# Kernel optimization log

Hardware: AMD Instinct MI355X
Metric: run time of the kernel (lower is better)

## Reference

```python
import jax, jax.numpy as jnp
import numpy as np


def setup_inputs() -> dict:
    key = jax.random.key(0)
    k1, k2, k3, k4, k5 = jax.random.split(key, 5)
    B, S, D, F, E = 4, 4096, 1024, 2048, 8
    top_k = 2
    num_tokens = B * S
    capacity = max(int(num_tokens / E * 1.25), 4)  # 2560
    scale = 0.02
    return {
        "x": jax.random.normal(k1, (B, S, D), dtype=jnp.float32),
        "gate_w": jax.random.normal(k2, (D, E), dtype=jnp.float32) * scale,
        "w_gate": jax.random.normal(k3, (E, D, F), dtype=jnp.float32) * scale,
        "w_up": jax.random.normal(k4, (E, D, F), dtype=jnp.float32) * scale,
        "w_down": jax.random.normal(k5, (E, F, D), dtype=jnp.float32) * scale,
        "num_experts": E,
        "top_k": top_k,
        "capacity": capacity,
    }


AUX_LOSS_WEIGHT = 0.01


def reference(x, gate_w, w_gate, w_up, w_down, num_experts, top_k, capacity):
    B, S, D = x.shape
    N = B * S
    x_flat = x.reshape(N, D)

    # ---- Router ----
    logits = x_flat @ gate_w                      # [N, E]
    probs = jax.nn.softmax(logits, axis=-1)
    weights, indices = jax.lax.top_k(probs, top_k)  # [N, K]
    weights = weights / jnp.sum(weights, axis=-1, keepdims=True)

    # ---- Capacity-based dispatch ----
    indices_flat = indices.reshape(-1)            # [N*K]
    x_rep = jnp.repeat(x_flat, top_k, axis=0)     # [N*K, D]
    expert_mask = jax.nn.one_hot(indices_flat, num_experts, dtype=jnp.int32)  # [N*K, E]
    token_priority = jnp.cumsum(expert_mask, axis=0) * expert_mask
    token_rank = jnp.sum(token_priority, axis=1)  # [N*K], 1-based rank within expert
    valid = (token_rank > 0) & (token_rank <= capacity)
    gather_idx = indices_flat * capacity + (token_rank - 1)  # [N*K]

    total_slots = num_experts * capacity
    # drop-mode scatter: invalid rows are sent out-of-bounds and dropped
    safe_idx = jnp.where(valid, gather_idx, total_slots)
    dispatched = jnp.zeros((total_slots, D), dtype=x.dtype)
    dispatched = dispatched.at[safe_idx].set(x_rep, mode="drop")
    dispatched = dispatched.reshape(num_experts, capacity, D)  # [E, C, D]

    # ---- Fused experts (grouped BMM, SwiGLU) ----
    gate = jnp.einsum("ecd,edf->ecf", dispatched, w_gate)
    up = jnp.einsum("ecd,edf->ecf", dispatched, w_up)
    hidden = jax.nn.silu(gate) * up
    expert_out = jnp.einsum("ecf,efd->ecd", hidden, w_down)
    expert_out_flat = expert_out.reshape(total_slots, D)

    # ---- Combine (row-aligned gather; dropped tokens contribute zero) ----
    gathered = expert_out_flat[jnp.clip(gather_idx, 0, total_slots - 1)]
    combined = jnp.where(valid[:, None], gathered, jnp.zeros((), dtype=x.dtype))
    combined = combined.reshape(N, top_k, D)
    output = jnp.sum(combined * weights[:, :, None], axis=1)  # [N, D]

    # ---- Aux load-balance loss ----
    mask = jax.nn.one_hot(indices, num_experts, dtype=jnp.float32).sum(axis=1)  # [N, E]
    f = mask.sum(axis=0) / (N * top_k + 1e-9)
    P = probs.mean(axis=0)
    aux_loss = num_experts * jnp.sum(f * P) * AUX_LOSS_WEIGHT

    return output.reshape(B, S, D), aux_loss
```

## Files before the change

### kernel.cpp

```cpp
#include <hip/hip_runtime.h>
#include <stdint.h>

#define N_TOK 16384
#define DIM   1024
#define NEXP  8
#define FF    2048
#define CAP   2560
#define NSLOT (NEXP*CAP)

using f32x4  = __attribute__((ext_vector_type(4))) float;
using bf16x8 = __attribute__((ext_vector_type(8))) short;

__device__ __forceinline__ unsigned short f2bf(float f){
  union { float f; unsigned u; } c; c.f = f;
  unsigned u = c.u + 0x7FFFu + ((c.u >> 16) & 1u);
  return (unsigned short)(u >> 16);
}
__device__ __forceinline__ float bf2f(unsigned short h){
  union { unsigned u; float f; } c; c.u = ((unsigned)h) << 16; return c.f;
}

__device__ __forceinline__ void gld16(const unsigned short* g, unsigned short* l){
  __builtin_amdgcn_global_load_lds((__attribute__((address_space(1))) void*)(void*)g,
                                   (__attribute__((address_space(3))) void*)l,
                                   16, 0, 0);
}

#define HBAR __builtin_amdgcn_s_barrier()
#define LG0  asm volatile("s_waitcnt lgkmcnt(0)" ::: "memory")

__global__ __launch_bounds__(256) void k_router(
    const float* __restrict__ x, const float* __restrict__ gate_w,
    int* __restrict__ topidx, float* __restrict__ topw,
    float* __restrict__ wavepart)
{
  __shared__ float gwT[NEXP][DIM];
  int tid = threadIdx.x;
  for (int i = tid; i < DIM*NEXP; i += 256) gwT[i & 7][i >> 3] = gate_w[i];
  __syncthreads();
  int wave = tid >> 6, lane = tid & 63;
  int t = blockIdx.x * 4 + wave;
  const float* xr = x + (size_t)t * DIM;
  double acc[NEXP];
  #pragma unroll
  for (int e = 0; e < NEXP; e++) acc[e] = 0.0;
  for (int j = 0; j < DIM/64; j++){
    double xv = (double)xr[lane + 64*j];
    #pragma unroll
    for (int e = 0; e < NEXP; e++) acc[e] += xv * (double)gwT[e][lane + 64*j];
  }
  #pragma unroll
  for (int off = 32; off >= 1; off >>= 1){
    #pragma unroll
    for (int e = 0; e < NEXP; e++) acc[e] += __shfl_xor(acc[e], off, 64);
  }
  if (lane == 0){
    double m = acc[0];
    #pragma unroll
    for (int e = 1; e < NEXP; e++) m = fmax(m, acc[e]);
    double p[NEXP], Z = 0.0;
    #pragma unroll
    for (int e = 0; e < NEXP; e++){ p[e] = exp(acc[e] - m); Z += p[e]; }
    double invZ = 1.0 / Z;
    #pragma unroll
    for (int e = 0; e < NEXP; e++) p[e] *= invZ;
    float4* wp = (float4*)(wavepart + (size_t)t*NEXP);
    wp[0] = make_float4((float)p[0], (float)p[1], (float)p[2], (float)p[3]);
    wp[1] = make_float4((float)p[4], (float)p[5], (float)p[6], (float)p[7]);
    int i0 = 0; double p0 = p[0];
    #pragma unroll
    for (int e = 1; e < NEXP; e++) if (p[e] > p0){ p0 = p[e]; i0 = e; }
    int i1 = (i0 == 0) ? 1 : 0; double p1 = p[i1];
    #pragma unroll
    for (int e = 0; e < NEXP; e++) if (e != i0 && p[e] > p1){ p1 = p[e]; i1 = e; }
    double s = p0 + p1;
    topidx[t*2+0] = i0; topidx[t*2+1] = i1;
    topw [t*2+0] = (float)(p0/s); topw[t*2+1] = (float)(p1/s);
  }
}

__global__ __launch_bounds__(1024) void k_scan_tcv(
    const int* __restrict__ topidx, const float* __restrict__ wavepart,
    int* __restrict__ slot_token, int* __restrict__ tok_slots,
    float* __restrict__ aux_out,
    const float* __restrict__ wg, const float* __restrict__ wu, const float* __restrict__ wd,
    unsigned short* __restrict__ B1, unsigned short* __restrict__ wdT)
{
  __shared__ uint8_t smem[32768];
  const int t = threadIdx.x;

  if (blockIdx.x == 0){
    int (*sc)[NEXP] = (int(*)[NEXP])smem;
    const int base_i = t * 32;
    int ids[32];
    #pragma unroll
    for (int j = 0; j < 32; j++) ids[j] = topidx[base_i + j];
    int b[NEXP];
    #pragma unroll
    for (int e = 0; e < NEXP; e++) b[e] = 0;
    #pragma unroll
    for (int j = 0; j < 32; j++){
      #pragma unroll
      for (int e = 0; e < NEXP; e++) if (ids[j] == e) b[e]++;
    }
    #pragma unroll
    for (int e = 0; e < NEXP; e++) sc[t][e] = b[e];
    __syncthreads();
    for (int off = 1; off < 1024; off <<= 1){
      int tmp[NEXP];
      #pragma unroll
      for (int e = 0; e < NEXP; e++) tmp[e] = (t >= off) ? sc[t-off][e] : 0;
      __syncthreads();
      #pragma unroll
      for (int e = 0; e < NEXP; e++) sc[t][e] += tmp[e];
      __syncthreads();
    }
    int myb[NEXP];
    #pragma unroll
    for (int e = 0; e < NEXP; e++) myb[e] = sc[t][e] - b[e];
    int cnt[NEXP];
    #pragma unroll
    for (int e = 0; e < NEXP; e++) cnt[e] = sc[1023][e];
    #pragma unroll
    for (int j = 0; j < 32; j++){
      int slot = -1;
      #pragma unroll
      for (int e = 0; e < NEXP; e++){
        if (ids[j] == e){
          int r = myb[e]; myb[e] = r + 1;
          if (r < CAP){
            slot = e*CAP + r;
            slot_token[slot] = (base_i + j) >> 1;
          }
        }
      }
      tok_slots[base_i + j] = slot;
    }
    __syncthreads();
    float pe[NEXP];
    #pragma unroll
    for (int e = 0; e < NEXP; e++) pe[e] = 0.f;
    for (int i = t; i < N_TOK; i += 1024){
      const float4* pr = (const float4*)(wavepart + (size_t)i*NEXP);
      float4 v0 = pr[0], v1 = pr[1];
      pe[0] += v0.x; pe[1] += v0.y; pe[2] += v0.z; pe[3] += v0.w;
      pe[4] += v1.x; pe[5] += v1.y; pe[6] += v1.z; pe[7] += v1.w;
    }
    #pragma unroll
    for (int off = 32; off >= 1; off >>= 1){
      #pragma unroll
      for (int e = 0; e < NEXP; e++) pe[e] += __shfl_xor(pe[e], off, 64);
    }
    __syncthreads();
    float* scf = (float*)smem;
    const int wv = t >> 6, ln = t & 63;
    if (ln == 0){
      #pragma unroll
      for (int e = 0; e < NEXP; e++) scf[wv*NEXP + e] = pe[e];
    }
    __syncthreads();
    if (t == 0){
      float aux = 0.f;
      #pragma unroll
      for (int e = 0; e < NEXP; e++){
        float P = 0.f;
        for (int w = 0; w < 16; w++) P += scf[w*NEXP + e];
        P /= (float)N_TOK;
        float f = (float)cnt[e] / ((float)(N_TOK*2) + 1e-9f);
        aux += f * P;
      }
      aux_out[0] = (float)NEXP * aux * 0.01f;
    }
  } else {
    float (*tt)[65] = (float(*)[65])smem;
    const int bid = blockIdx.x - 1;
    const int z = bid >> 9, rem = bid & 511;
    const int mode = z >> 3, e = z & 7;
    const float* in; unsigned short* out; int R, C, ct, rt;
    if (mode < 2){
      in  = (mode == 0 ? wg : wu) + (size_t)e * DIM * FF;
      out = B1 + (size_t)e * 2 * FF * DIM;
      R = DIM; C = FF; ct = rem & 31; rt = rem >> 5;
    } else {
      in  = wd + (size_t)e * FF * DIM;
      out = wdT + (size_t)e * DIM * FF;
      R = FF; C = DIM; ct = rem >> 5; rt = rem & 31;
    }
    const int c0 = ct * 64, r0 = rt * 64;
    {
      int row = t >> 4, c4 = t & 15;
      float4 v = *(const float4*)(in + (size_t)(r0 + row)*C + c0 + c4*4);
      tt[c4*4+0][row] = v.x; tt[c4*4+1][row] = v.y;
      tt[c4*4+2][row] = v.z; tt[c4*4+3][row] = v.w;
    }
    __syncthreads();
    {
      int cl = t >> 4;
      int rs = (t & 15) * 4;
      int c  = c0 + cl;
      int orow = (mode == 0) ? ((c>>4)*32 + (c&15))
               : (mode == 1) ? ((c>>4)*32 + 16 + (c&15))
               : c;
      unsigned long long pk = 0;
      #pragma unroll
      for (int j = 0; j < 4; j++) pk |= (unsigned long long)f2bf(tt[cl][rs+j]) << (16*j);
      *(unsigned long long*)(out + (size_t)orow*R + r0 + rs) = pk;
    }
  }
}

__global__ __launch_bounds__(256) void k_gather(
    const float* __restrict__ x, const int* __restrict__ slot_token,
    unsigned short* __restrict__ disp)
{
  const int s = blockIdx.x;
  const int t = slot_token[s];
  const int tid = threadIdx.x;
  unsigned long long pk = 0ull;
  if (t >= 0){
    float4 v = *(const float4*)(x + (size_t)t*DIM + tid*4);
    pk =  (unsigned long long)f2bf(v.x)
       | ((unsigned long long)f2bf(v.y) << 16)
       | ((unsigned long long)f2bf(v.z) << 32)
       | ((unsigned long long)f2bf(v.w) << 48);
  }
  *(unsigned long long*)(disp + (size_t)s*DIM + tid*4) = pk;
}

__device__ __forceinline__ void stg(const unsigned short* gsrc, int ldg,
                                    unsigned short* Lh, int wave, int lane){
  const int sl = (lane & 3) ^ ((lane >> 3) & 3);
  #pragma unroll
  for (int j = 0; j < 2; j++){
    int bi = wave*2 + j;
    gld16(gsrc + (size_t)(bi*16 + (lane >> 2))*ldg + sl*8, Lh + bi*512);
  }
}
__device__ __forceinline__ bf16x8 frd(const unsigned short* Lh, int r, int g){
  return *(const bf16x8*)(Lh + r*32 + (((g ^ ((r >> 1) & 3))) << 3));
}
template<int MG>
__device__ __forceinline__ void mm16(f32x4 (&acc)[8][4], const bf16x8 (&a)[4], const bf16x8 (&b)[4]){
  #pragma unroll
  for (int i = 0; i < 4; i++)
    #pragma unroll
    for (int n = 0; n < 4; n++)
      acc[MG*4+i][n] = __builtin_amdgcn_mfma_f32_16x16x32_bf16(a[i], b[n], acc[MG*4+i][n], 0, 0, 0);
}

#define HALF_STEP(RS, DOSTG, VMW, ASRC, BSRC)                                   \
  {                                                                             \
    unsigned short* LA = lds + (RS)*16384;                                      \
    unsigned short* LB = LA + 8192;                                             \
    unsigned short* NS = lds + (((RS)+3)&3)*16384;                              \
    bf16x8 a[4], b[4];                                                          \
    _Pragma("unroll")                                                           \
    for (int i = 0; i < 4; i++) a[i] = frd(LA, wr*128 + i*16 + l15, g);         \
    _Pragma("unroll")                                                           \
    for (int n = 0; n < 4; n++) b[n] = frd(LB, wc*64 + n*16 + l15, g);          \
    if (DOSTG) stg(ASRC, LDG, NS, wave, lane);                                  \
    HBAR; LG0;                                                                  \
    __builtin_amdgcn_s_setprio(1);  mm16<0>(acc, a, b);                         \
    __builtin_amdgcn_s_setprio(0);                                              \
    HBAR;                                                                       \
    _Pragma("unroll")                                                           \
    for (int i = 0; i < 4; i++) a[i] = frd(LA, wr*128 + (4+i)*16 + l15, g);     \
    if (DOSTG) stg(BSRC, LDG, NS + 8192, wave, lane);                           \
    HBAR; LG0;                                                                  \
    __builtin_amdgcn_s_setprio(1);  mm16<1>(acc, a, b);                         \
    __builtin_amdgcn_s_setprio(0);                                              \
    if ((VMW) == 4) { asm volatile("s_waitcnt vmcnt(4)" ::: "memory"); }        \
    else if ((VMW) == 0) { asm volatile("s_waitcnt vmcnt(0)" ::: "memory"); }   \
    HBAR;                                                                       \
  }

template<int KDIM, int LDG, int EPI>
__global__ __launch_bounds__(512, 2) void k_gemm8(
    const unsigned short* __restrict__ A,
    const unsigned short* __restrict__ B,
    unsigned short* __restrict__ Out0,
    unsigned short* __restrict__ Out1)
{
  constexpr int NH    = KDIM / 32;
  constexpr int BROWS = (EPI == 1) ? 2*FF : DIM;
  constexpr int LDO   = (EPI == 1) ? FF : DIM;
  __shared__ unsigned short lds[65536];
  const int id = blockIdx.x;
  const int e  = id & 7;
  int t  = id >> 3;
  int ks = 0;
  if (EPI == 2){ ks = t & 1; t >>= 1; }
  const int mt = t % 10, nt = t / 10;
  const int m0 = mt*256, n0 = nt*256;
  const unsigned short* Ab = A + ((size_t)e*CAP   + m0) * LDG + (size_t)ks*KDIM;
  const unsigned short* Bb = B + ((size_t)e*BROWS + n0) * LDG + (size_t)ks*KDIM;
  const int tid = threadIdx.x, wave = tid >> 6, lane = tid & 63;
  const int wr = wave >> 2, wc = wave & 3;
  const int g = lane >> 4, l15 = lane & 15;

  f32x4 acc[8][4];
  const f32x4 z4 = {0.f,0.f,0.f,0.f};
  #pragma unroll
  for (int i = 0; i < 8; i++)
    #pragma unroll
    for (int n = 0; n < 4; n++) acc[i][n] = z4;

  stg(Ab,      LDG, lds + 0*16384,        wave, lane);
  stg(Bb,      LDG, lds + 0*16384 + 8192, wave, lane);
  stg(Ab + 32, LDG, lds + 1*16384,        wave, lane);
  stg(Bb + 32, LDG, lds + 1*16384 + 8192, wave, lane);
  stg(Ab + 64, LDG, lds + 2*16384,        wave, lane);
  stg(Bb + 64, LDG, lds + 2*16384 + 8192, wave, lane);
  asm volatile("s_waitcnt vmcnt(4)" ::: "memory");
  HBAR;

  for (int h = 0; h + 8 <= NH; h += 4){
    HALF_STEP(0, true, -1, Ab + (size_t)(h+3)*32, Bb + (size_t)(h+3)*32);
    HALF_STEP(1, true,  4, Ab + (size_t)(h+4)*32, Bb + (size_t)(h+4)*32);
    HALF_STEP(2, true, -1, Ab + (size_t)(h+5)*32, Bb + (size_t)(h+5)*32);
    HALF_STEP(3, true,  4, Ab + (size_t)(h+6)*32, Bb + (size_t)(h+6)*32);
  }
  HALF_STEP(0, true, -1, Ab + (size_t)(NH-1)*32, Bb + (size_t)(NH-1)*32);
  HALF_STEP(1, false, 0, Ab, Bb);
  HALF_STEP(2, false, -1, Ab, Bb);
  HALF_STEP(3, false, -1, Ab, Bb);

  if (EPI == 1){
    unsigned short* H = Out0 + ((size_t)e*CAP + m0 + wr*128) * (size_t)LDO;
    const int hc0 = (n0 + wc*64) >> 1;
    #pragma unroll
    for (int mf = 0; mf < 8; mf++)
      #pragma unroll
      for (int q = 0; q < 4; q++){
        int r = mf*16 + g*4 + q;
        #pragma unroll
        for (int p = 0; p < 2; p++){
          float gg = acc[mf][2*p][q], uu = acc[mf][2*p+1][q];
          float h = gg / (1.f + __expf(-gg)) * uu;
          H[(size_t)r*LDO + hc0 + p*16 + l15] = f2bf(h);
        }
      }
  } else {
    unsigned short* P = (ks ? Out1 : Out0);
    unsigned short* O = P + ((size_t)e*CAP + m0 + wr*128) * (size_t)LDO + n0 + wc*64;
    #pragma unroll
    for (int mf = 0; mf < 8; mf++)
      #pragma unroll
      for (int q = 0; q < 4; q++){
        int r = mf*16 + g*4 + q;
        #pragma unroll
        for (int n = 0; n < 4; n++)
          O[(size_t)r*LDO + n*16 + l15] = f2bf(acc[mf][n][q]);
      }
  }
}

__global__ __launch_bounds__(256) void k_combine(
    const unsigned short* __restrict__ P0, const unsigned short* __restrict__ P1,
    const int* __restrict__ tok_slots, const float* __restrict__ topw,
    float* __restrict__ out)
{
  const int t = blockIdx.x*2 + (threadIdx.x >> 7);
  const int tid = threadIdx.x & 127;
  const int s0 = tok_slots[t*2+0], s1 = tok_slots[t*2+1];
  const float w0 = topw[t*2+0], w1 = topw[t*2+1];
  float r[8];
  #pragma unroll
  for (int j = 0; j < 8; j++) r[j] = 0.f;
  if (s0 >= 0){
    bf16x8 v0 = *(const bf16x8*)(P0 + (size_t)s0*DIM + tid*8);
    bf16x8 v1 = *(const bf16x8*)(P1 + (size_t)s0*DIM + tid*8);
    #pragma unroll
    for (int j = 0; j < 8; j++)
      r[j] += w0 * (bf2f((unsigned short)v0[j]) + bf2f((unsigned short)v1[j]));
  }
  if (s1 >= 0){
    bf16x8 v0 = *(const bf16x8*)(P0 + (size_t)s1*DIM + tid*8);
    bf16x8 v1 = *(const bf16x8*)(P1 + (size_t)s1*DIM + tid*8);
    #pragma unroll
    for (int j = 0; j < 8; j++)
      r[j] += w1 * (bf2f((unsigned short)v0[j]) + bf2f((unsigned short)v1[j]));
  }
  float4* o = (float4*)(out + (size_t)t*DIM + tid*8);
  o[0] = make_float4(r[0], r[1], r[2], r[3]);
  o[1] = make_float4(r[4], r[5], r[6], r[7]);
}

extern "C" void kernel_launch(void* const* d_in, const int* in_sizes, int n_in,
                              void* d_out, int out_size, void* d_ws, size_t ws_size,
                              hipStream_t stream)
{
  const float* x      = (const float*)d_in[0];
  const float* gate_w = (const float*)d_in[1];
  const float* w_gate = (const float*)d_in[2];
  const float* w_up   = (const float*)d_in[3];
  const float* w_down = (const float*)d_in[4];
  float* out = (float*)d_out;

  uint8_t* ws = (uint8_t*)d_ws;
  int*   topidx       = (int*)ws;               ws += (size_t)N_TOK*2*4;
  float* topw         = (float*)ws;             ws += (size_t)N_TOK*2*4;
  int*   slot_token   = (int*)ws;               ws += (size_t)NSLOT*4;
  int*   tok_slots    = (int*)ws;               ws += (size_t)N_TOK*2*4;
  float* wavepart     = (float*)ws;             ws += (size_t)N_TOK*NEXP*4;
  unsigned short* disp   = (unsigned short*)ws; ws += (size_t)NSLOT*DIM*2;
  unsigned short* hidden = (unsigned short*)ws; ws += (size_t)NSLOT*FF*2;
  unsigned short* B1     = (unsigned short*)ws; ws += (size_t)NEXP*2*FF*DIM*2;
  unsigned short* wdT    = (unsigned short*)ws; ws += (size_t)NEXP*DIM*FF*2;
  size_t need = (size_t)(ws - (uint8_t*)d_ws);
  if (ws_size < need) return;
  unsigned short* P0 = disp;
  unsigned short* P1 = B1;

  hipMemsetAsync(slot_token, 0xFF, (size_t)NSLOT * sizeof(int), stream);

  k_router<<<N_TOK/4, 256, 0, stream>>>(x, gate_w, topidx, topw, wavepart);
  k_scan_tcv<<<12289, 1024, 0, stream>>>(topidx, wavepart, slot_token, tok_slots,
                                         out + (size_t)N_TOK*DIM,
                                         w_gate, w_up, w_down, B1, wdT);
  k_gather<<<NSLOT, 256, 0, stream>>>(x, slot_token, disp);
  k_gemm8<DIM, DIM, 1><<<1280, 512, 0, stream>>>(disp, B1, hidden, nullptr);
  k_gemm8<DIM, FF, 2><<<640, 512, 0, stream>>>(hidden, wdT, P0, P1);
  k_combine<<<N_TOK/2, 256, 0, stream>>>(P0, P1, tok_slots, topw, out);
}
```

Baseline: 440.8 us.

## Fuse token gather into first GEMM via indirect A loads from bf16 x

Removes the separate gather kernel and the memset. x is converted once to bf16 by extra blocks of the scan/transpose kernel, and the first expert GEMM loads A rows straight from that buffer through per-row token indices read from slot_token. Unused slots are marked -1 inside the scan block and clamped to token 0. Those rows still get computed but are never combined. This saves writing and re-reading the dispatched buffer, at the cost of scattered row loads in the GEMM A-staging path.

Measured after the change: 435.9 us. About the same (-1.1%).

```diff
diff --git a/kernel.cpp b/kernel.cpp
--- a/kernel.cpp
+++ b/kernel.cpp
@@ -84,12 +84,14 @@
     int* __restrict__ slot_token, int* __restrict__ tok_slots,
     float* __restrict__ aux_out,
     const float* __restrict__ wg, const float* __restrict__ wu, const float* __restrict__ wd,
-    unsigned short* __restrict__ B1, unsigned short* __restrict__ wdT)
+    unsigned short* __restrict__ B1, unsigned short* __restrict__ wdT,
+    const float* __restrict__ x, unsigned short* __restrict__ xb)
 {
   __shared__ uint8_t smem[32768];
   const int t = threadIdx.x;
-
-  if (blockIdx.x == 0){
+  const int bidx = blockIdx.x;
+
+  if (bidx == 0){
     int (*sc)[NEXP] = (int(*)[NEXP])smem;
     const int base_i = t * 32;
     int ids[32];
@@ -136,6 +138,10 @@
       }
       tok_slots[base_i + j] = slot;
     }
+    for (int idx = t; idx < NSLOT; idx += 1024){
+      int e2 = idx / CAP, r2 = idx - e2*CAP;
+      if (r2 >= cnt[e2]) slot_token[idx] = -1;
+    }
     __syncthreads();
     float pe[NEXP];
     #pragma unroll
@@ -171,9 +177,9 @@
       }
       aux_out[0] = (float)NEXP * aux * 0.01f;
     }
-  } else {
+  } else if (bidx <= 12288){
     float (*tt)[65] = (float(*)[65])smem;
-    const int bid = blockIdx.x - 1;
+    const int bid = bidx - 1;
     const int z = bid >> 9, rem = bid & 511;
     const int mode = z >> 3, e = z & 7;
     const float* in; unsigned short* out; int R, C, ct, rt;
@@ -206,25 +212,17 @@
       for (int j = 0; j < 4; j++) pk |= (unsigned long long)f2bf(tt[cl][rs+j]) << (16*j);
       *(unsigned long long*)(out + (size_t)orow*R + r0 + rs) = pk;
     }
-  }
-}
-
-__global__ __launch_bounds__(256) void k_gather(
-    const float* __restrict__ x, const int* __restrict__ slot_token,
-    unsigned short* __restrict__ disp)
-{
-  const int s = blockIdx.x;
-  const int t = slot_token[s];
-  const int tid = threadIdx.x;
-  unsigned long long pk = 0ull;
-  if (t >= 0){
-    float4 v = *(const float4*)(x + (size_t)t*DIM + tid*4);
-    pk =  (unsigned long long)f2bf(v.x)
-       | ((unsigned long long)f2bf(v.y) << 16)
-       | ((unsigned long long)f2bf(v.z) << 32)
-       | ((unsigned long long)f2bf(v.w) << 48);
-  }
-  *(unsigned long long*)(disp + (size_t)s*DIM + tid*4) = pk;
+  } else {
+    const int gb = bidx - 12289;
+    size_t base = ((size_t)gb*1024 + t)*4;
+    float4 v = *(const float4*)(x + base);
+    unsigned long long pk =
+        (unsigned long long)f2bf(v.x)
+      | ((unsigned long long)f2bf(v.y) << 16)
+      | ((unsigned long long)f2bf(v.z) << 32)
+      | ((unsigned long long)f2bf(v.w) << 48);
+    *(unsigned long long*)(xb + base) = pk;
+  }
 }
 
 __device__ __forceinline__ void stg(const unsigned short* gsrc, int ldg,
@@ -236,6 +234,12 @@
     gld16(gsrc + (size_t)(bi*16 + (lane >> 2))*ldg + sl*8, Lh + bi*512);
   }
 }
+__device__ __forceinline__ void stgA_ind(const unsigned short* xb, int tok0, int tok1, int k0,
+                                         unsigned short* Lh, int wave, int lane){
+  const int sl = (lane & 3) ^ ((lane >> 3) & 3);
+  gld16(xb + (size_t)tok0*DIM + k0 + sl*8, Lh + (wave*2+0)*512);
+  gld16(xb + (size_t)tok1*DIM + k0 + sl*8, Lh + (wave*2+1)*512);
+}
 __device__ __forceinline__ bf16x8 frd(const unsigned short* Lh, int r, int g){
   return *(const bf16x8*)(Lh + r*32 + (((g ^ ((r >> 1) & 3))) << 3));
 }
@@ -248,7 +252,11 @@
       acc[MG*4+i][n] = __builtin_amdgcn_mfma_f32_16x16x32_bf16(a[i], b[n], acc[MG*4+i][n], 0, 0, 0);
 }
 
-#define HALF_STEP(RS, DOSTG, VMW, ASRC, BSRC)                                   \
+#define STG_A(HH, NS)                                                           \
+  { if (EPI == 1) stgA_ind(A, tokA0, tokA1, (HH)*32, NS, wave, lane);           \
+    else          stg(Ab + (size_t)(HH)*32, LDG, NS, wave, lane); }
+
+#define HALF_STEP(RS, DOSTG, VMW, HH)                                           \
   {                                                                             \
     unsigned short* LA = lds + (RS)*16384;                                      \
     unsigned short* LB = LA + 8192;                                             \
@@ -258,14 +266,14 @@
     for (int i = 0; i < 4; i++) a[i] = frd(LA, wr*128 + i*16 + l15, g);         \
     _Pragma("unroll")                                                           \
     for (int n = 0; n < 4; n++) b[n] = frd(LB, wc*64 + n*16 + l15, g);          \
-    if (DOSTG) stg(ASRC, LDG, NS, wave, lane);                                  \
+    if (DOSTG) STG_A(HH, NS);                                                   \
     HBAR; LG0;                                                                  \
     __builtin_amdgcn_s_setprio(1);  mm16<0>(acc, a, b);                         \
     __builtin_amdgcn_s_setprio(0);                                              \
     HBAR;                                                                       \
     _Pragma("unroll")                                                           \
     for (int i = 0; i < 4; i++) a[i] = frd(LA, wr*128 + (4+i)*16 + l15, g);     \
-    if (DOSTG) stg(BSRC, LDG, NS + 8192, wave, lane);                           \
+    if (DOSTG) stg(Bb + (size_t)(HH)*32, LDG, NS + 8192, wave, lane);           \
     HBAR; LG0;                                                                  \
     __builtin_amdgcn_s_setprio(1);  mm16<1>(acc, a, b);                         \
     __builtin_amdgcn_s_setprio(0);                                              \
@@ -279,7 +287,8 @@
     const unsigned short* __restrict__ A,
     const unsigned short* __restrict__ B,
     unsigned short* __restrict__ Out0,
-    unsigned short* __restrict__ Out1)
+    unsigned short* __restrict__ Out1,
+    const int* __restrict__ slot_token)
 {
   constexpr int NH    = KDIM / 32;
   constexpr int BROWS = (EPI == 1) ? 2*FF : DIM;
@@ -298,6 +307,16 @@
   const int wr = wave >> 2, wc = wave & 3;
   const int g = lane >> 4, l15 = lane & 15;
 
+  int tokA0 = 0, tokA1 = 0;
+  if (EPI == 1){
+    int r0 = m0 + (wave*2+0)*16 + (lane >> 2);
+    int r1 = m0 + (wave*2+1)*16 + (lane >> 2);
+    int t0 = slot_token[e*CAP + r0];
+    int t1 = slot_token[e*CAP + r1];
+    tokA0 = (t0 < 0) ? 0 : t0;
+    tokA1 = (t1 < 0) ? 0 : t1;
+  }
+
   f32x4 acc[8][4];
   const f32x4 z4 = {0.f,0.f,0.f,0.f};
   #pragma unroll
@@ -305,25 +324,25 @@
     #pragma unroll
     for (int n = 0; n < 4; n++) acc[i][n] = z4;
 
-  stg(Ab,      LDG, lds + 0*16384,        wave, lane);
+  STG_A(0, lds + 0*16384);
   stg(Bb,      LDG, lds + 0*16384 + 8192, wave, lane);
-  stg(Ab + 32, LDG, lds + 1*16384,        wave, lane);
+  STG_A(1, lds + 1*16384);
   stg(Bb + 32, LDG, lds + 1*16384 + 8192, wave, lane);
-  stg(Ab + 64, LDG, lds + 2*16384,        wave, lane);
+  STG_A(2, lds + 2*16384);
   stg(Bb + 64, LDG, lds + 2*16384 + 8192, wave, lane);
   asm volatile("s_waitcnt vmcnt(4)" ::: "memory");
   HBAR;
 
   for (int h = 0; h + 8 <= NH; h += 4){
-    HALF_STEP(0, true, -1, Ab + (size_t)(h+3)*32, Bb + (size_t)(h+3)*32);
-    HALF_STEP(1, true,  4, Ab + (size_t)(h+4)*32, Bb + (size_t)(h+4)*32);
-    HALF_STEP(2, true, -1, Ab + (size_t)(h+5)*32, Bb + (size_t)(h+5)*32);
-    HALF_STEP(3, true,  4, Ab + (size_t)(h+6)*32, Bb + (size_t)(h+6)*32);
-  }
-  HALF_STEP(0, true, -1, Ab + (size_t)(NH-1)*32, Bb + (size_t)(NH-1)*32);
-  HALF_STEP(1, false, 0, Ab, Bb);
-  HALF_STEP(2, false, -1, Ab, Bb);
-  HALF_STEP(3, false, -1, Ab, Bb);
+    HALF_STEP(0, true, -1, h+3);
+    HALF_STEP(1, true,  4, h+4);
+    HALF_STEP(2, true, -1, h+5);
+    HALF_STEP(3, true,  4, h+6);
+  }
+  HALF_STEP(0, true, -1, NH-1);
+  HALF_STEP(1, false, 0, 0);
+  HALF_STEP(2, false, -1, 0);
+  HALF_STEP(3, false, -1, 0);
 
   if (EPI == 1){
     unsigned short* H = Out0 + ((size_t)e*CAP + m0 + wr*128) * (size_t)LDO;
@@ -403,23 +422,20 @@
   int*   slot_token   = (int*)ws;               ws += (size_t)NSLOT*4;
   int*   tok_slots    = (int*)ws;               ws += (size_t)N_TOK*2*4;
   float* wavepart     = (float*)ws;             ws += (size_t)N_TOK*NEXP*4;
-  unsigned short* disp   = (unsigned short*)ws; ws += (size_t)NSLOT*DIM*2;
+  unsigned short* xb     = (unsigned short*)ws; ws += (size_t)N_TOK*DIM*2;
+  unsigned short* P0     = (unsigned short*)ws; ws += (size_t)NSLOT*DIM*2;
   unsigned short* hidden = (unsigned short*)ws; ws += (size_t)NSLOT*FF*2;
   unsigned short* B1     = (unsigned short*)ws; ws += (size_t)NEXP*2*FF*DIM*2;
   unsigned short* wdT    = (unsigned short*)ws; ws += (size_t)NEXP*DIM*FF*2;
   size_t need = (size_t)(ws - (uint8_t*)d_ws);
   if (ws_size < need) return;
-  unsigned short* P0 = disp;
   unsigned short* P1 = B1;
 
-  hipMemsetAsync(slot_token, 0xFF, (size_t)NSLOT * sizeof(int), stream);
-
   k_router<<<N_TOK/4, 256, 0, stream>>>(x, gate_w, topidx, topw, wavepart);
-  k_scan_tcv<<<12289, 1024, 0, stream>>>(topidx, wavepart, slot_token, tok_slots,
+  k_scan_tcv<<<16385, 1024, 0, stream>>>(topidx, wavepart, slot_token, tok_slots,
                                          out + (size_t)N_TOK*DIM,
-                                         w_gate, w_up, w_down, B1, wdT);
-  k_gather<<<NSLOT, 256, 0, stream>>>(x, slot_token, disp);
-  k_gemm8<DIM, DIM, 1><<<1280, 512, 0, stream>>>(disp, B1, hidden, nullptr);
-  k_gemm8<DIM, FF, 2><<<640, 512, 0, stream>>>(hidden, wdT, P0, P1);
+                                         w_gate, w_up, w_down, B1, wdT, x, xb);
+  k_gemm8<DIM, DIM, 1><<<1280, 512, 0, stream>>>(xb, B1, hidden, nullptr, slot_token);
+  k_gemm8<DIM, FF, 2><<<640, 512, 0, stream>>>(hidden, wdT, P0, P1, nullptr);
   k_combine<<<N_TOK/2, 256, 0, stream>>>(P0, P1, tok_slots, topw, out);
 }
```
